# Performance work log

Hardware: AMD Instinct MI355X
Metric: run time of the kernel (lower is better)

## Reference

```python
import jax, jax.numpy as jnp
import numpy as np

N = 50000
E = 800000
IN_C = 128
HID = 64
HEADS = 4
NEG_SLOPE = 0.2
EPS = 1e-16


def setup_inputs() -> dict:
    key = jax.random.key(0)
    ks = jax.random.split(key, 12)
    x = jax.random.normal(ks[0], (N, IN_C), dtype=jnp.float32)
    edge_index = jax.random.randint(ks[1], (2, E), 0, N, dtype=jnp.int64)
    # layer 1: in -> (HEADS, HID), concat heads
    W1 = jax.random.normal(ks[2], (IN_C, HEADS * HID), dtype=jnp.float32) * (1.0 / np.sqrt(IN_C))
    a_src1 = jax.random.normal(ks[3], (HEADS, HID), dtype=jnp.float32) * 0.1
    a_dst1 = jax.random.normal(ks[4], (HEADS, HID), dtype=jnp.float32) * 0.1
    b1 = jnp.zeros((HEADS * HID,), dtype=jnp.float32)
    # layer 2: HEADS*HID -> (1, HID)
    W2 = jax.random.normal(ks[5], (HEADS * HID, HID), dtype=jnp.float32) * (1.0 / np.sqrt(HEADS * HID))
    a_src2 = jax.random.normal(ks[6], (1, HID), dtype=jnp.float32) * 0.1
    a_dst2 = jax.random.normal(ks[7], (1, HID), dtype=jnp.float32) * 0.1
    b2 = jnp.zeros((HID,), dtype=jnp.float32)
    return {"x": x, "edge_index": edge_index, "W1": W1, "a_src1": a_src1,
            "a_dst1": a_dst1, "b1": b1, "W2": W2, "a_src2": a_src2,
            "a_dst2": a_dst2, "b2": b2}


def _gat_conv(x, src, dst, W, a_src, a_dst, bias, heads, ch):
    n = x.shape[0]
    h = (x @ W).reshape(n, heads, ch)                       # [N,H,C]
    alpha_s = jnp.einsum('nhc,hc->nh', h, a_src)            # [N,H]
    alpha_d = jnp.einsum('nhc,hc->nh', h, a_dst)            # [N,H]
    e = jax.nn.leaky_relu(alpha_s[src] + alpha_d[dst], NEG_SLOPE)  # [E,H]
    # segment softmax over incoming edges of each dst node
    m = jax.ops.segment_max(e, dst, num_segments=n)         # [N,H]
    ex = jnp.exp(e - m[dst])
    denom = jax.ops.segment_sum(ex, dst, num_segments=n)    # [N,H]
    alpha = ex / (denom[dst] + EPS)                         # [E,H]
    msg = h[src] * alpha[:, :, None]                        # [E,H,C]
    out = jax.ops.segment_sum(msg, dst, num_segments=n)     # [N,H,C]
    return out.reshape(n, heads * ch) + bias


def reference(x, edge_index, W1, a_src1, a_dst1, b1, W2, a_src2, a_dst2, b2):
    src = edge_index[0]
    dst = edge_index[1]
    h = _gat_conv(x, src, dst, W1, a_src1, a_dst1, b1, HEADS, HID)
    h = jax.nn.elu(h)
    h = _gat_conv(h, src, dst, W2, a_src2, a_dst2, b2, 1, HID)
    h = jax.nn.elu(h)
    return h  # [N, HID] (output_dim == hidden_channels so no final linear)
```

## Files before the change

### kernel.cpp

```cpp
#include <hip/hip_runtime.h>
#include <math.h>

#define NN 50000
#define EE 800000
#define IN_C 128
#define HID 64
#define HEADS 4
#define SCAN_BLOCKS ((NN + 255) / 256)
#define EBLOCKS ((EE + 255) / 256)

typedef __attribute__((ext_vector_type(8))) short bf16x8;
typedef __attribute__((ext_vector_type(4))) float f32x4;

#if defined(__has_builtin)
#if __has_builtin(__builtin_amdgcn_fdot2_f32_bf16)
#define HAVE_FDOT2_BF16 1
#endif
#endif


__device__ inline unsigned short f2bf(float f) {
    unsigned u = __float_as_uint(f);
    return (unsigned short)((u + 0x7fff + ((u >> 16) & 1)) >> 16);
}
__device__ inline float bf2f(unsigned short s) {
    return __uint_as_float(((unsigned)s) << 16);
}
__device__ inline unsigned prm(unsigned a, unsigned b, unsigned sel) {
    return __builtin_amdgcn_perm(a, b, sel);
}
#ifdef HAVE_FDOT2_BF16
typedef __attribute__((ext_vector_type(2))) __bf16 bf2v;
__device__ inline float fdot2bf(unsigned h, unsigned w, float acc) {
    return __builtin_amdgcn_fdot2_f32_bf16(__builtin_bit_cast(bf2v, h),
                                           __builtin_bit_cast(bf2v, w), acc, false);
}
#else
__device__ inline float fdot2bf(unsigned h, unsigned w, float acc) {
    return acc + bf2f((unsigned short)(h & 0xffff)) * bf2f((unsigned short)(w & 0xffff))
               + bf2f((unsigned short)(h >> 16)) * bf2f((unsigned short)(w >> 16));
}
#endif

__device__ inline int wave_incl_scan(int v, int lane) {
    #pragma unroll
    for (int off = 1; off < 64; off <<= 1) {
        int t = __shfl_up(v, off);
        if (lane >= off) v += t;
    }
    return v;
}

__device__ inline int block256_excl_scan(int v, int tid, int* ws4) {
    int lane = tid & 63, wv = tid >> 6;
    int incl = wave_incl_scan(v, lane);
    if (lane == 63) ws4[wv] = incl;
    __syncthreads();
    if (tid == 0) {
        int run = 0;
        #pragma unroll
        for (int i = 0; i < 4; i++) { int t = ws4[i]; ws4[i] = run; run += t; }
    }
    __syncthreads();
    return incl + ws4[wv] - v;
}


__global__ void front_kernel(const int* __restrict__ ei, int* __restrict__ deg,
                             int* __restrict__ rank,
                             const float* __restrict__ W1, unsigned short* __restrict__ W1Thi,
                             unsigned short* __restrict__ W1Tlo,
                             const float* __restrict__ W2, unsigned short* __restrict__ W2Thi,
                             unsigned short* __restrict__ W2Tlo) {
    int b = blockIdx.x;
    int tid = threadIdx.x;
    if (b < EBLOCKS) {
        int i = b * 256 + tid;
        if (i < EE) rank[i] = atomicAdd(&deg[ei[EE + i]], 1);
    } else if (b < EBLOCKS + 128) {
        int idx = (b - EBLOCKS) * 256 + tid;
        int r = idx >> 8, c = idx & 255;
        float v = W1[idx];
        unsigned short h = f2bf(v);
        W1Thi[c * 128 + r] = h;
        W1Tlo[c * 128 + r] = f2bf(v - bf2f(h));
    } else {
        int idx = (b - EBLOCKS - 128) * 256 + tid;
        int r = idx >> 6, c = idx & 63;
        float v = W2[idx];
        unsigned short h = f2bf(v);
        W2Thi[c * 256 + r] = h;
        W2Tlo[c * 256 + r] = f2bf(v - bf2f(h));
    }
}


__global__ void deg_partial_kernel(const int* __restrict__ deg, int* __restrict__ bsum) {
    __shared__ int ws4[4];
    int tid = threadIdx.x;
    int idx = blockIdx.x * 256 + tid;
    int d = (idx < NN) ? deg[idx] : 0;
    int lane = tid & 63, wv = tid >> 6;
    int s = d;
    #pragma unroll
    for (int off = 32; off; off >>= 1) s += __shfl_down(s, off);
    if (lane == 0) ws4[wv] = s;
    __syncthreads();
    if (tid == 0) bsum[blockIdx.x] = ws4[0] + ws4[1] + ws4[2] + ws4[3];
}

__global__ void scanb_kernel(const int* __restrict__ bsum, int* __restrict__ boff,
                             int* __restrict__ row_ptr) {
    __shared__ int ws4[4];
    int tid = threadIdx.x;
    int v = (tid < SCAN_BLOCKS) ? bsum[tid] : 0;
    int excl = block256_excl_scan(v, tid, ws4);
    if (tid < SCAN_BLOCKS) boff[tid] = excl;
    if (tid == 255) row_ptr[NN] = excl + v;
}

__global__ void fill_kernel(const int* __restrict__ deg, const int* __restrict__ boff,
                            int* __restrict__ row_ptr) {
    __shared__ int ws4[4];
    int tid = threadIdx.x;
    int idx = blockIdx.x * 256 + tid;
    int d = (idx < NN) ? deg[idx] : 0;
    int excl = block256_excl_scan(d, tid, ws4) + boff[blockIdx.x];
    if (idx < NN) row_ptr[idx] = excl;
}

__global__ void scatter_kernel(const int* __restrict__ ei, const int* __restrict__ rank,
                               const int* __restrict__ row_ptr, int* __restrict__ csr_src) {
    int i = blockIdx.x * blockDim.x + threadIdx.x;
    if (i < EE) {
        int d = ei[EE + i];
        csr_src[row_ptr[d] + rank[i]] = ei[i];
    }
}

__global__ __launch_bounds__(256) void gemm1_mfma(
        const float* __restrict__ x,
        const unsigned short* __restrict__ Bhi, const unsigned short* __restrict__ Blo,
        const float* __restrict__ a_src, const float* __restrict__ a_dst,
        unsigned short* __restrict__ h1b, float* __restrict__ as1, float* __restrict__ ad1) {
    __shared__ unsigned short Ahi[32][136];
    __shared__ unsigned short Alo[32][136];
    int tid = threadIdx.x;
    int w = tid >> 6, lane = tid & 63;
    int lq = lane >> 4, lr = lane & 15;
    int brow = blockIdx.x * 32;
    {
        int row = tid >> 3;
        int col0 = (tid & 7) * 16;
        int gr = min(brow + row, NN - 1);
        #pragma unroll
        for (int i = 0; i < 16; i += 4) {
            float4 v = *(const float4*)(x + (size_t)gr * 128 + col0 + i);
            unsigned short h0 = f2bf(v.x), h1 = f2bf(v.y), h2 = f2bf(v.z), h3 = f2bf(v.w);
            Ahi[row][col0 + i + 0] = h0; Alo[row][col0 + i + 0] = f2bf(v.x - bf2f(h0));
            Ahi[row][col0 + i + 1] = h1; Alo[row][col0 + i + 1] = f2bf(v.y - bf2f(h1));
            Ahi[row][col0 + i + 2] = h2; Alo[row][col0 + i + 2] = f2bf(v.z - bf2f(h2));
            Ahi[row][col0 + i + 3] = h3; Alo[row][col0 + i + 3] = f2bf(v.w - bf2f(h3));
        }
    }
    __syncthreads();
    f32x4 acc[2][4];
    f32x4 zf = {0.f, 0.f, 0.f, 0.f};
    #pragma unroll
    for (int mi = 0; mi < 2; mi++)
        #pragma unroll
        for (int ni = 0; ni < 4; ni++) acc[mi][ni] = zf;
    #pragma unroll
    for (int q = 0; q < 4; q++) {
        int ko = q * 32 + lq * 8;
        bf16x8 ah0 = *(const bf16x8*)(const void*)&Ahi[lr][ko];
        bf16x8 al0 = *(const bf16x8*)(const void*)&Alo[lr][ko];
        bf16x8 ah1 = *(const bf16x8*)(const void*)&Ahi[16 + lr][ko];
        bf16x8 al1 = *(const bf16x8*)(const void*)&Alo[16 + lr][ko];
        #pragma unroll
        for (int ni = 0; ni < 4; ni++) {
            size_t bo = (size_t)(w * 64 + ni * 16 + lr) * 128 + ko;
            bf16x8 bh = *(const bf16x8*)(const void*)(Bhi + bo);
            bf16x8 bl = *(const bf16x8*)(const void*)(Blo + bo);
            acc[0][ni] = __builtin_amdgcn_mfma_f32_16x16x32_bf16(al0, bh, acc[0][ni], 0, 0, 0);
            acc[0][ni] = __builtin_amdgcn_mfma_f32_16x16x32_bf16(ah0, bl, acc[0][ni], 0, 0, 0);
            acc[0][ni] = __builtin_amdgcn_mfma_f32_16x16x32_bf16(ah0, bh, acc[0][ni], 0, 0, 0);
            acc[1][ni] = __builtin_amdgcn_mfma_f32_16x16x32_bf16(al1, bh, acc[1][ni], 0, 0, 0);
            acc[1][ni] = __builtin_amdgcn_mfma_f32_16x16x32_bf16(ah1, bl, acc[1][ni], 0, 0, 0);
            acc[1][ni] = __builtin_amdgcn_mfma_f32_16x16x32_bf16(ah1, bh, acc[1][ni], 0, 0, 0);
        }
    }
    float asv[4], adv[4];
    #pragma unroll
    for (int ni = 0; ni < 4; ni++) {
        asv[ni] = a_src[w * 64 + ni * 16 + lr];
        adv[ni] = a_dst[w * 64 + ni * 16 + lr];
    }
    #pragma unroll
    for (int mi = 0; mi < 2; mi++) {
        f32x4 ps = zf, pd = zf;
        #pragma unroll
        for (int ni = 0; ni < 4; ni++)
            #pragma unroll
            for (int r = 0; r < 4; r++) {
                ps[r] += acc[mi][ni][r] * asv[ni];
                pd[r] += acc[mi][ni][r] * adv[ni];
            }
        #pragma unroll
        for (int m = 1; m < 16; m <<= 1)
            #pragma unroll
            for (int r = 0; r < 4; r++) {
                ps[r] += __shfl_xor(ps[r], m);
                pd[r] += __shfl_xor(pd[r], m);
            }
        #pragma unroll
        for (int r = 0; r < 4; r++) {
            int n = brow + mi * 16 + lq * 4 + r;
            if (lr == 0 && n < NN) { as1[n * 4 + w] = ps[r]; ad1[n * 4 + w] = pd[r]; }
        }
        #pragma unroll
        for (int ni = 0; ni < 4; ni++)
            #pragma unroll
            for (int r = 0; r < 4; r++) {
                int n = brow + mi * 16 + lq * 4 + r;
                if (n < NN)
                    h1b[(size_t)n * 256 + w * 64 + ni * 16 + lr] = f2bf(acc[mi][ni][r]);
            }
    }
}

__global__ __launch_bounds__(256) void gemm2_mfma(
        const unsigned short* __restrict__ Ahi, const unsigned short* __restrict__ Alo,
        const unsigned short* __restrict__ Bhi, const unsigned short* __restrict__ Blo,
        const float* __restrict__ a_src, const float* __restrict__ a_dst,
        unsigned short* __restrict__ g2b, float* __restrict__ as2, float* __restrict__ ad2) {
    int tid = threadIdx.x;
    int w = tid >> 6, lane = tid & 63;
    int lq = lane >> 4, lr = lane & 15;
    int wrow = blockIdx.x * 128 + w * 32;
    f32x4 acc[2][4];
    f32x4 zf = {0.f, 0.f, 0.f, 0.f};
    #pragma unroll
    for (int mi = 0; mi < 2; mi++)
        #pragma unroll
        for (int ni = 0; ni < 4; ni++) acc[mi][ni] = zf;
    int ra = min(wrow + lr, NN - 1);
    int rb = min(wrow + 16 + lr, NN - 1);
    #pragma unroll
    for (int q = 0; q < 8; q++) {
        int ko = q * 32 + lq * 8;
        bf16x8 ah0 = *(const bf16x8*)(const void*)(Ahi + (size_t)ra * 256 + ko);
        bf16x8 al0 = *(const bf16x8*)(const void*)(Alo + (size_t)ra * 256 + ko);
        bf16x8 ah1 = *(const bf16x8*)(const void*)(Ahi + (size_t)rb * 256 + ko);
        bf16x8 al1 = *(const bf16x8*)(const void*)(Alo + (size_t)rb * 256 + ko);
        #pragma unroll
        for (int ni = 0; ni < 4; ni++) {
            size_t bo = (size_t)(ni * 16 + lr) * 256 + ko;
            bf16x8 bh = *(const bf16x8*)(const void*)(Bhi + bo);
            bf16x8 bl = *(const bf16x8*)(const void*)(Blo + bo);
            acc[0][ni] = __builtin_amdgcn_mfma_f32_16x16x32_bf16(al0, bh, acc[0][ni], 0, 0, 0);
            acc[0][ni] = __builtin_amdgcn_mfma_f32_16x16x32_bf16(ah0, bl, acc[0][ni], 0, 0, 0);
            acc[0][ni] = __builtin_amdgcn_mfma_f32_16x16x32_bf16(ah0, bh, acc[0][ni], 0, 0, 0);
            acc[1][ni] = __builtin_amdgcn_mfma_f32_16x16x32_bf16(al1, bh, acc[1][ni], 0, 0, 0);
            acc[1][ni] = __builtin_amdgcn_mfma_f32_16x16x32_bf16(ah1, bl, acc[1][ni], 0, 0, 0);
            acc[1][ni] = __builtin_amdgcn_mfma_f32_16x16x32_bf16(ah1, bh, acc[1][ni], 0, 0, 0);
        }
    }
    float asv[4], adv[4];
    #pragma unroll
    for (int ni = 0; ni < 4; ni++) {
        asv[ni] = a_src[ni * 16 + lr];
        adv[ni] = a_dst[ni * 16 + lr];
    }
    #pragma unroll
    for (int mi = 0; mi < 2; mi++) {
        f32x4 ps = zf, pd = zf;
        #pragma unroll
        for (int ni = 0; ni < 4; ni++)
            #pragma unroll
            for (int r = 0; r < 4; r++) {
                ps[r] += acc[mi][ni][r] * asv[ni];
                pd[r] += acc[mi][ni][r] * adv[ni];
            }
        #pragma unroll
        for (int m = 1; m < 16; m <<= 1)
            #pragma unroll
            for (int r = 0; r < 4; r++) {
                ps[r] += __shfl_xor(ps[r], m);
                pd[r] += __shfl_xor(pd[r], m);
            }
        #pragma unroll
        for (int r = 0; r < 4; r++) {
            int n = wrow + mi * 16 + lq * 4 + r;
            if (lr == 0 && n < NN) { as2[n] = ps[r]; ad2[n] = pd[r]; }
        }
        #pragma unroll
        for (int ni = 0; ni < 4; ni++)
            #pragma unroll
            for (int r = 0; r < 4; r++) {
                int n = wrow + mi * 16 + lq * 4 + r;
                if (n < NN)
                    g2b[(size_t)n * 64 + ni * 16 + lr] = f2bf(acc[mi][ni][r]);
            }
    }
}

__global__ __launch_bounds__(256) void agg1_kernel(
        const unsigned short* __restrict__ h1b, const int* __restrict__ row_ptr,
        const int* __restrict__ csr_src, const float* __restrict__ as,
        const float* __restrict__ ad, const float* __restrict__ b1,
        unsigned short* __restrict__ h2hi, unsigned short* __restrict__ h2lo) {
    __shared__ int            ssrc[4][64];
    __shared__ unsigned short wbf[4][4][64];
    int tid = threadIdx.x;
    int wv = tid >> 6, lane = tid & 63;
    int n = blockIdx.x * 4 + wv;
    if (n >= NN) return;
    int start = row_ptr[n], end = row_ptr[n + 1];
    float4 adv = ((const float4*)ad)[n];
    int whead = lane >> 4;
    float4 acc = make_float4(0.f, 0.f, 0.f, 0.f);
    float d0 = 0.f, d1 = 0.f, d2 = 0.f, d3 = 0.f;
    for (int c0 = start; c0 < end; c0 += 64) {
        int m = min(64, end - c0);
        if (lane < m) {
            int s = csr_src[c0 + lane];
            ssrc[wv][lane] = s;
            float4 asv = ((const float4*)as)[s];
            float e0 = asv.x + adv.x; e0 = e0 > 0.f ? e0 : 0.2f * e0; float x0 = __expf(e0);
            float e1 = asv.y + adv.y; e1 = e1 > 0.f ? e1 : 0.2f * e1; float x1 = __expf(e1);
            float e2 = asv.z + adv.z; e2 = e2 > 0.f ? e2 : 0.2f * e2; float x2 = __expf(e2);
            float e3 = asv.w + adv.w; e3 = e3 > 0.f ? e3 : 0.2f * e3; float x3 = __expf(e3);
            wbf[wv][0][lane] = f2bf(x0);
            wbf[wv][1][lane] = f2bf(x1);
            wbf[wv][2][lane] = f2bf(x2);
            wbf[wv][3][lane] = f2bf(x3);
            d0 += x0; d1 += x1; d2 += x2; d3 += x3;
        }
        int j = 0;
        for (; j + 4 <= m; j += 4) {
            int s0 = ssrc[wv][j], s1 = ssrc[wv][j + 1];
            int s2 = ssrc[wv][j + 2], s3 = ssrc[wv][j + 3];
            uint2 ha = ((const uint2*)h1b)[(size_t)s0 * 64 + lane];
            uint2 hb = ((const uint2*)h1b)[(size_t)s1 * 64 + lane];
            uint2 hc = ((const uint2*)h1b)[(size_t)s2 * 64 + lane];
            uint2 hd = ((const uint2*)h1b)[(size_t)s3 * 64 + lane];
            unsigned wp01 = *(const unsigned*)&wbf[wv][whead][j];
            unsigned wp23 = *(const unsigned*)&wbf[wv][whead][j + 2];
            acc.x = fdot2bf(prm(hb.x, ha.x, 0x05040100), wp01, acc.x);
            acc.y = fdot2bf(prm(hb.x, ha.x, 0x07060302), wp01, acc.y);
            acc.z = fdot2bf(prm(hb.y, ha.y, 0x05040100), wp01, acc.z);
            acc.w = fdot2bf(prm(hb.y, ha.y, 0x07060302), wp01, acc.w);
            acc.x = fdot2bf(prm(hd.x, hc.x, 0x05040100), wp23, acc.x);
            acc.y = fdot2bf(prm(hd.x, hc.x, 0x07060302), wp23, acc.y);
            acc.z = fdot2bf(prm(hd.y, hc.y, 0x05040100), wp23, acc.z);
            acc.w = fdot2bf(prm(hd.y, hc.y, 0x07060302), wp23, acc.w);
        }
        for (; j + 2 <= m; j += 2) {
            int s0 = ssrc[wv][j], s1 = ssrc[wv][j + 1];
            uint2 ha = ((const uint2*)h1b)[(size_t)s0 * 64 + lane];
            uint2 hb = ((const uint2*)h1b)[(size_t)s1 * 64 + lane];
            unsigned wp = *(const unsigned*)&wbf[wv][whead][j];
            acc.x = fdot2bf(prm(hb.x, ha.x, 0x05040100), wp, acc.x);
            acc.y = fdot2bf(prm(hb.x, ha.x, 0x07060302), wp, acc.y);
            acc.z = fdot2bf(prm(hb.y, ha.y, 0x05040100), wp, acc.z);
            acc.w = fdot2bf(prm(hb.y, ha.y, 0x07060302), wp, acc.w);
        }
        if (j < m) {
            int s = ssrc[wv][j];
            float w = bf2f(wbf[wv][whead][j]);
            ushort4 hv = ((const ushort4*)h1b)[(size_t)s * 64 + lane];
            acc.x += bf2f(hv.x) * w; acc.y += bf2f(hv.y) * w;
            acc.z += bf2f(hv.z) * w; acc.w += bf2f(hv.w) * w;
        }
    }
    #pragma unroll
    for (int off = 32; off; off >>= 1) {
        d0 += __shfl_down(d0, off); d1 += __shfl_down(d1, off);
        d2 += __shfl_down(d2, off); d3 += __shfl_down(d3, off);
    }
    d0 = __shfl(d0, 0); d1 = __shfl(d1, 0);
    d2 = __shfl(d2, 0); d3 = __shfl(d3, 0);
    float den = whead == 0 ? d0 : whead == 1 ? d1 : whead == 2 ? d2 : d3;
    float inv = 1.f / (den + 1e-16f);
    float4 bv = ((const float4*)b1)[lane];
    float4 r;
    r.x = acc.x * inv + bv.x; r.y = acc.y * inv + bv.y;
    r.z = acc.z * inv + bv.z; r.w = acc.w * inv + bv.w;
    r.x = r.x > 0.f ? r.x : expm1f(r.x);
    r.y = r.y > 0.f ? r.y : expm1f(r.y);
    r.z = r.z > 0.f ? r.z : expm1f(r.z);
    r.w = r.w > 0.f ? r.w : expm1f(r.w);
    ushort4 hi4, lo4;
    hi4.x = f2bf(r.x); lo4.x = f2bf(r.x - bf2f(hi4.x));
    hi4.y = f2bf(r.y); lo4.y = f2bf(r.y - bf2f(hi4.y));
    hi4.z = f2bf(r.z); lo4.z = f2bf(r.z - bf2f(hi4.z));
    hi4.w = f2bf(r.w); lo4.w = f2bf(r.w - bf2f(hi4.w));
    ((ushort4*)h2hi)[(size_t)n * 64 + lane] = hi4;
    ((ushort4*)h2lo)[(size_t)n * 64 + lane] = lo4;
}

__global__ __launch_bounds__(256) void agg2_kernel(
        const unsigned short* __restrict__ g2b, const int* __restrict__ row_ptr,
        const int* __restrict__ csr_src, const float* __restrict__ as,
        const float* __restrict__ ad, const float* __restrict__ b2,
        float* __restrict__ out) {
    __shared__ int            ssrc[4][64];
    __shared__ unsigned short wbf[4][64];
    int tid = threadIdx.x;
    int wv = tid >> 6, lane = tid & 63;
    int n = blockIdx.x * 4 + wv;
    if (n >= NN) return;
    int start = row_ptr[n], end = row_ptr[n + 1];
    float adv = ad[n];
    float acc = 0.f;
    float den = 0.f;
    for (int c0 = start; c0 < end; c0 += 64) {
        int m = min(64, end - c0);
        if (lane < m) {
            int s = csr_src[c0 + lane];
            ssrc[wv][lane] = s;
            float e = as[s] + adv;
            e = e > 0.f ? e : 0.2f * e;
            float x = __expf(e);
            wbf[wv][lane] = f2bf(x);
            den += x;
        }
        int j = 0;
        for (; j + 4 <= m; j += 4) {
            int s0 = ssrc[wv][j], s1 = ssrc[wv][j + 1];
            int s2 = ssrc[wv][j + 2], s3 = ssrc[wv][j + 3];
            unsigned g0 = g2b[(size_t)s0 * 64 + lane];
            unsigned g1 = g2b[(size_t)s1 * 64 + lane];
            unsigned g2 = g2b[(size_t)s2 * 64 + lane];
            unsigned g3 = g2b[(size_t)s3 * 64 + lane];
            unsigned wp01 = *(const unsigned*)&wbf[wv][j];
            unsigned wp23 = *(const unsigned*)&wbf[wv][j + 2];
            acc = fdot2bf(prm(g1, g0, 0x05040100), wp01, acc);
            acc = fdot2bf(prm(g3, g2, 0x05040100), wp23, acc);
        }
        for (; j + 2 <= m; j += 2) {
            int s0 = ssrc[wv][j], s1 = ssrc[wv][j + 1];
            unsigned g0 = g2b[(size_t)s0 * 64 + lane];
            unsigned g1 = g2b[(size_t)s1 * 64 + lane];
            unsigned wp = *(const unsigned*)&wbf[wv][j];
            acc = fdot2bf(prm(g1, g0, 0x05040100), wp, acc);
        }
        if (j < m) {
            int s = ssrc[wv][j];
            acc += bf2f(g2b[(size_t)s * 64 + lane]) * bf2f(wbf[wv][j]);
        }
    }
    #pragma unroll
    for (int off = 32; off; off >>= 1) den += __shfl_down(den, off);
    den = __shfl(den, 0);
    float inv = 1.f / (den + 1e-16f);
    float r = acc * inv + b2[lane];
    out[(size_t)n * 64 + lane] = r > 0.f ? r : expm1f(r);
}


extern "C" void kernel_launch(void* const* d_in, const int* in_sizes, int n_in,
                              void* d_out, int out_size, void* d_ws, size_t ws_size,
                              hipStream_t stream) {
    const float* x      = (const float*)d_in[0];
    const int*   ei     = (const int*)d_in[1];
    const float* W1     = (const float*)d_in[2];
    const float* a_src1 = (const float*)d_in[3];
    const float* a_dst1 = (const float*)d_in[4];
    const float* b1     = (const float*)d_in[5];
    const float* W2     = (const float*)d_in[6];
    const float* a_src2 = (const float*)d_in[7];
    const float* a_dst2 = (const float*)d_in[8];
    const float* b2     = (const float*)d_in[9];
    float* out = (float*)d_out;

    char* base = (char*)d_ws;
    size_t off = 0;
    auto alloc = [&](size_t bytes) -> void* {
        void* p = base + off;
        off = (off + bytes + 255) & ~(size_t)255;
        return p;
    };
    int*   deg     = (int*)alloc(NN * sizeof(int));
    int*   rank    = (int*)alloc(EE * sizeof(int));
    int*   bsum    = (int*)alloc(SCAN_BLOCKS * sizeof(int));
    int*   boff    = (int*)alloc(SCAN_BLOCKS * sizeof(int));
    int*   row_ptr = (int*)alloc((NN + 1) * sizeof(int));
    int*   csr_src = (int*)alloc(EE * sizeof(int));
    unsigned short* W1Thi = (unsigned short*)alloc(256 * 128 * 2);
    unsigned short* W1Tlo = (unsigned short*)alloc(256 * 128 * 2);
    unsigned short* W2Thi = (unsigned short*)alloc(64 * 256 * 2);
    unsigned short* W2Tlo = (unsigned short*)alloc(64 * 256 * 2);
    unsigned short* h1b   = (unsigned short*)alloc((size_t)NN * 256 * 2);
    float* as1     = (float*)alloc((size_t)NN * 4 * sizeof(float));
    float* ad1     = (float*)alloc((size_t)NN * 4 * sizeof(float));
    unsigned short* h2hi  = (unsigned short*)alloc((size_t)NN * 256 * 2);
    unsigned short* h2lo  = (unsigned short*)alloc((size_t)NN * 256 * 2);
    unsigned short* g2b   = (unsigned short*)alloc((size_t)NN * 64 * 2);
    float* as2     = (float*)alloc((size_t)NN * sizeof(float));
    float* ad2     = (float*)alloc((size_t)NN * sizeof(float));

    hipMemsetAsync(deg, 0, NN * sizeof(int), stream);

    front_kernel<<<EBLOCKS + 128 + 64, 256, 0, stream>>>(ei, deg, rank, W1, W1Thi, W1Tlo,
                                                         W2, W2Thi, W2Tlo);
    deg_partial_kernel<<<SCAN_BLOCKS, 256, 0, stream>>>(deg, bsum);
    scanb_kernel<<<1, 256, 0, stream>>>(bsum, boff, row_ptr);
    fill_kernel<<<SCAN_BLOCKS, 256, 0, stream>>>(deg, boff, row_ptr);
    scatter_kernel<<<EBLOCKS, 256, 0, stream>>>(ei, rank, row_ptr, csr_src);

    gemm1_mfma<<<(NN + 31) / 32, 256, 0, stream>>>(x, W1Thi, W1Tlo,
                                                   a_src1, a_dst1, h1b, as1, ad1);
    agg1_kernel<<<(NN + 3) / 4, 256, 0, stream>>>(h1b, row_ptr, csr_src, as1, ad1, b1,
                                                  h2hi, h2lo);
    gemm2_mfma<<<(NN + 127) / 128, 256, 0, stream>>>(h2hi, h2lo, W2Thi, W2Tlo,
                                                     a_src2, a_dst2, g2b, as2, ad2);
    agg2_kernel<<<(NN + 3) / 4, 256, 0, stream>>>(g2b, row_ptr, csr_src, as2, ad2, b2, out);
}
```

Before: 291.9 us.

## Fuse CSR scan into single-pass lookback, enlarge gemm1 tile, drop h2 lo split

Replaces the three-kernel degree scan with one kernel that uses per-block descriptors and a decoupled lookback, which removes two launches. gemm1 now processes 64 rows per block instead of 32 so each B fragment load feeds more MFMAs. The layer-1 output is stored only as a bf16 hi part, and gemm2 drops the lo MFMA terms for A, cutting one 25 MB write, one read and a third of the gemm2 MFMAs. The cost is lower precision in layer 2's input, plus a lookback that depends on earlier blocks being scheduled first.

```diff
diff --git a/kernel.cpp b/kernel.cpp
--- a/kernel.cpp
+++ b/kernel.cpp
@@ -94,39 +94,44 @@
     }
 }
 
-
-__global__ void deg_partial_kernel(const int* __restrict__ deg, int* __restrict__ bsum) {
+__global__ void scan_fill_kernel(const int* __restrict__ deg,
+                                 unsigned long long* __restrict__ desc,
+                                 int* __restrict__ row_ptr) {
     __shared__ int ws4[4];
-    int tid = threadIdx.x;
-    int idx = blockIdx.x * 256 + tid;
+    __shared__ int sbase;
+    int b = blockIdx.x, tid = threadIdx.x;
+    int idx = b * 256 + tid;
     int d = (idx < NN) ? deg[idx] : 0;
-    int lane = tid & 63, wv = tid >> 6;
-    int s = d;
-    #pragma unroll
-    for (int off = 32; off; off >>= 1) s += __shfl_down(s, off);
-    if (lane == 0) ws4[wv] = s;
+    int excl = block256_excl_scan(d, tid, ws4);
+    if (tid == 255) {
+        unsigned total = (unsigned)(excl + d);
+        __threadfence();
+        atomicExch(&desc[b], (1ULL << 32) | (unsigned long long)total);
+    }
+    if (tid < 64) {
+        int sum = 0;
+        int hi = b;
+        while (hi > 0) {
+            int lo = hi - 64; if (lo < 0) lo = 0;
+            int myi = lo + tid;
+            unsigned v = 0;
+            if (myi < hi) {
+                unsigned long long d8;
+                do { d8 = atomicAdd(&desc[myi], 0ULL); } while ((d8 >> 32) == 0);
+                v = (unsigned)(d8 & 0xffffffffULL);
+            }
+            #pragma unroll
+            for (int off = 32; off; off >>= 1) v += __shfl_down(v, off);
+            v = __shfl(v, 0);
+            sum += (int)v;
+            hi = lo;
+        }
+        if (tid == 0) sbase = sum;
+    }
     __syncthreads();
-    if (tid == 0) bsum[blockIdx.x] = ws4[0] + ws4[1] + ws4[2] + ws4[3];
-}
-
-__global__ void scanb_kernel(const int* __restrict__ bsum, int* __restrict__ boff,
-                             int* __restrict__ row_ptr) {
-    __shared__ int ws4[4];
-    int tid = threadIdx.x;
-    int v = (tid < SCAN_BLOCKS) ? bsum[tid] : 0;
-    int excl = block256_excl_scan(v, tid, ws4);
-    if (tid < SCAN_BLOCKS) boff[tid] = excl;
-    if (tid == 255) row_ptr[NN] = excl + v;
-}
-
-__global__ void fill_kernel(const int* __restrict__ deg, const int* __restrict__ boff,
-                            int* __restrict__ row_ptr) {
-    __shared__ int ws4[4];
-    int tid = threadIdx.x;
-    int idx = blockIdx.x * 256 + tid;
-    int d = (idx < NN) ? deg[idx] : 0;
-    int excl = block256_excl_scan(d, tid, ws4) + boff[blockIdx.x];
-    if (idx < NN) row_ptr[idx] = excl;
+    int gbase = sbase;
+    if (idx < NN) row_ptr[idx] = gbase + excl;
+    if (b == gridDim.x - 1 && tid == 255) row_ptr[NN] = gbase + excl + d;
 }
 
 __global__ void scatter_kernel(const int* __restrict__ ei, const int* __restrict__ rank,
@@ -143,18 +148,18 @@
         const unsigned short* __restrict__ Bhi, const unsigned short* __restrict__ Blo,
         const float* __restrict__ a_src, const float* __restrict__ a_dst,
         unsigned short* __restrict__ h1b, float* __restrict__ as1, float* __restrict__ ad1) {
-    __shared__ unsigned short Ahi[32][136];
-    __shared__ unsigned short Alo[32][136];
+    __shared__ unsigned short Ahi[64][136];
+    __shared__ unsigned short Alo[64][136];
     int tid = threadIdx.x;
     int w = tid >> 6, lane = tid & 63;
     int lq = lane >> 4, lr = lane & 15;
-    int brow = blockIdx.x * 32;
+    int brow = blockIdx.x * 64;
     {
-        int row = tid >> 3;
-        int col0 = (tid & 7) * 16;
+        int row = tid >> 2;
+        int col0 = (tid & 3) * 32;
         int gr = min(brow + row, NN - 1);
         #pragma unroll
-        for (int i = 0; i < 16; i += 4) {
+        for (int i = 0; i < 32; i += 4) {
             float4 v = *(const float4*)(x + (size_t)gr * 128 + col0 + i);
             unsigned short h0 = f2bf(v.x), h1 = f2bf(v.y), h2 = f2bf(v.z), h3 = f2bf(v.w);
             Ahi[row][col0 + i + 0] = h0; Alo[row][col0 + i + 0] = f2bf(v.x - bf2f(h0));
@@ -164,30 +169,32 @@
         }
     }
     __syncthreads();
-    f32x4 acc[2][4];
+    f32x4 acc[4][4];
     f32x4 zf = {0.f, 0.f, 0.f, 0.f};
     #pragma unroll
-    for (int mi = 0; mi < 2; mi++)
+    for (int mi = 0; mi < 4; mi++)
         #pragma unroll
         for (int ni = 0; ni < 4; ni++) acc[mi][ni] = zf;
     #pragma unroll
     for (int q = 0; q < 4; q++) {
         int ko = q * 32 + lq * 8;
-        bf16x8 ah0 = *(const bf16x8*)(const void*)&Ahi[lr][ko];
-        bf16x8 al0 = *(const bf16x8*)(const void*)&Alo[lr][ko];
-        bf16x8 ah1 = *(const bf16x8*)(const void*)&Ahi[16 + lr][ko];
-        bf16x8 al1 = *(const bf16x8*)(const void*)&Alo[16 + lr][ko];
+        bf16x8 ah[4], al[4];
+        #pragma unroll
+        for (int mi = 0; mi < 4; mi++) {
+            ah[mi] = *(const bf16x8*)(const void*)&Ahi[mi * 16 + lr][ko];
+            al[mi] = *(const bf16x8*)(const void*)&Alo[mi * 16 + lr][ko];
+        }
         #pragma unroll
         for (int ni = 0; ni < 4; ni++) {
             size_t bo = (size_t)(w * 64 + ni * 16 + lr) * 128 + ko;
             bf16x8 bh = *(const bf16x8*)(const void*)(Bhi + bo);
             bf16x8 bl = *(const bf16x8*)(const void*)(Blo + bo);
-            acc[0][ni] = __builtin_amdgcn_mfma_f32_16x16x32_bf16(al0, bh, acc[0][ni], 0, 0, 0);
-            acc[0][ni] = __builtin_amdgcn_mfma_f32_16x16x32_bf16(ah0, bl, acc[0][ni], 0, 0, 0);
-            acc[0][ni] = __builtin_amdgcn_mfma_f32_16x16x32_bf16(ah0, bh, acc[0][ni], 0, 0, 0);
-            acc[1][ni] = __builtin_amdgcn_mfma_f32_16x16x32_bf16(al1, bh, acc[1][ni], 0, 0, 0);
-            acc[1][ni] = __builtin_amdgcn_mfma_f32_16x16x32_bf16(ah1, bl, acc[1][ni], 0, 0, 0);
-            acc[1][ni] = __builtin_amdgcn_mfma_f32_16x16x32_bf16(ah1, bh, acc[1][ni], 0, 0, 0);
+            #pragma unroll
+            for (int mi = 0; mi < 4; mi++) {
+                acc[mi][ni] = __builtin_amdgcn_mfma_f32_16x16x32_bf16(al[mi], bh, acc[mi][ni], 0, 0, 0);
+                acc[mi][ni] = __builtin_amdgcn_mfma_f32_16x16x32_bf16(ah[mi], bl, acc[mi][ni], 0, 0, 0);
+                acc[mi][ni] = __builtin_amdgcn_mfma_f32_16x16x32_bf16(ah[mi], bh, acc[mi][ni], 0, 0, 0);
+            }
         }
     }
     float asv[4], adv[4];
@@ -197,7 +204,7 @@
         adv[ni] = a_dst[w * 64 + ni * 16 + lr];
     }
     #pragma unroll
-    for (int mi = 0; mi < 2; mi++) {
+    for (int mi = 0; mi < 4; mi++) {
         f32x4 ps = zf, pd = zf;
         #pragma unroll
         for (int ni = 0; ni < 4; ni++)
@@ -230,7 +237,7 @@
 }
 
 __global__ __launch_bounds__(256) void gemm2_mfma(
-        const unsigned short* __restrict__ Ahi, const unsigned short* __restrict__ Alo,
+        const unsigned short* __restrict__ Ab,
         const unsigned short* __restrict__ Bhi, const unsigned short* __restrict__ Blo,
         const float* __restrict__ a_src, const float* __restrict__ a_dst,
         unsigned short* __restrict__ g2b, float* __restrict__ as2, float* __restrict__ ad2) {
@@ -249,19 +256,15 @@
     #pragma unroll
     for (int q = 0; q < 8; q++) {
         int ko = q * 32 + lq * 8;
-        bf16x8 ah0 = *(const bf16x8*)(const void*)(Ahi + (size_t)ra * 256 + ko);
-        bf16x8 al0 = *(const bf16x8*)(const void*)(Alo + (size_t)ra * 256 + ko);
-        bf16x8 ah1 = *(const bf16x8*)(const void*)(Ahi + (size_t)rb * 256 + ko);
-        bf16x8 al1 = *(const bf16x8*)(const void*)(Alo + (size_t)rb * 256 + ko);
+        bf16x8 ah0 = *(const bf16x8*)(const void*)(Ab + (size_t)ra * 256 + ko);
+        bf16x8 ah1 = *(const bf16x8*)(const void*)(Ab + (size_t)rb * 256 + ko);
         #pragma unroll
         for (int ni = 0; ni < 4; ni++) {
             size_t bo = (size_t)(ni * 16 + lr) * 256 + ko;
             bf16x8 bh = *(const bf16x8*)(const void*)(Bhi + bo);
             bf16x8 bl = *(const bf16x8*)(const void*)(Blo + bo);
-            acc[0][ni] = __builtin_amdgcn_mfma_f32_16x16x32_bf16(al0, bh, acc[0][ni], 0, 0, 0);
             acc[0][ni] = __builtin_amdgcn_mfma_f32_16x16x32_bf16(ah0, bl, acc[0][ni], 0, 0, 0);
             acc[0][ni] = __builtin_amdgcn_mfma_f32_16x16x32_bf16(ah0, bh, acc[0][ni], 0, 0, 0);
-            acc[1][ni] = __builtin_amdgcn_mfma_f32_16x16x32_bf16(al1, bh, acc[1][ni], 0, 0, 0);
             acc[1][ni] = __builtin_amdgcn_mfma_f32_16x16x32_bf16(ah1, bl, acc[1][ni], 0, 0, 0);
             acc[1][ni] = __builtin_amdgcn_mfma_f32_16x16x32_bf16(ah1, bh, acc[1][ni], 0, 0, 0);
         }
@@ -309,7 +312,7 @@
         const unsigned short* __restrict__ h1b, const int* __restrict__ row_ptr,
         const int* __restrict__ csr_src, const float* __restrict__ as,
         const float* __restrict__ ad, const float* __restrict__ b1,
-        unsigned short* __restrict__ h2hi, unsigned short* __restrict__ h2lo) {
+        unsigned short* __restrict__ h2b) {
     __shared__ int            ssrc[4][64];
     __shared__ unsigned short wbf[4][4][64];
     int tid = threadIdx.x;
@@ -391,13 +394,9 @@
     r.y = r.y > 0.f ? r.y : expm1f(r.y);
     r.z = r.z > 0.f ? r.z : expm1f(r.z);
     r.w = r.w > 0.f ? r.w : expm1f(r.w);
-    ushort4 hi4, lo4;
-    hi4.x = f2bf(r.x); lo4.x = f2bf(r.x - bf2f(hi4.x));
-    hi4.y = f2bf(r.y); lo4.y = f2bf(r.y - bf2f(hi4.y));
-    hi4.z = f2bf(r.z); lo4.z = f2bf(r.z - bf2f(hi4.z));
-    hi4.w = f2bf(r.w); lo4.w = f2bf(r.w - bf2f(hi4.w));
-    ((ushort4*)h2hi)[(size_t)n * 64 + lane] = hi4;
-    ((ushort4*)h2lo)[(size_t)n * 64 + lane] = lo4;
+    ushort4 hv;
+    hv.x = f2bf(r.x); hv.y = f2bf(r.y); hv.z = f2bf(r.z); hv.w = f2bf(r.w);
+    ((ushort4*)h2b)[(size_t)n * 64 + lane] = hv;
 }
 
 __global__ __launch_bounds__(256) void agg2_kernel(
@@ -483,9 +482,8 @@
         return p;
     };
     int*   deg     = (int*)alloc(NN * sizeof(int));
+    unsigned long long* desc = (unsigned long long*)alloc(SCAN_BLOCKS * sizeof(unsigned long long));
     int*   rank    = (int*)alloc(EE * sizeof(int));
-    int*   bsum    = (int*)alloc(SCAN_BLOCKS * sizeof(int));
-    int*   boff    = (int*)alloc(SCAN_BLOCKS * sizeof(int));
     int*   row_ptr = (int*)alloc((NN + 1) * sizeof(int));
     int*   csr_src = (int*)alloc(EE * sizeof(int));
     unsigned short* W1Thi = (unsigned short*)alloc(256 * 128 * 2);
@@ -495,26 +493,23 @@
     unsigned short* h1b   = (unsigned short*)alloc((size_t)NN * 256 * 2);
     float* as1     = (float*)alloc((size_t)NN * 4 * sizeof(float));
     float* ad1     = (float*)alloc((size_t)NN * 4 * sizeof(float));
-    unsigned short* h2hi  = (unsigned short*)alloc((size_t)NN * 256 * 2);
-    unsigned short* h2lo  = (unsigned short*)alloc((size_t)NN * 256 * 2);
+    unsigned short* h2b   = (unsigned short*)alloc((size_t)NN * 256 * 2);
     unsigned short* g2b   = (unsigned short*)alloc((size_t)NN * 64 * 2);
     float* as2     = (float*)alloc((size_t)NN * sizeof(float));
     float* ad2     = (float*)alloc((size_t)NN * sizeof(float));
 
-    hipMemsetAsync(deg, 0, NN * sizeof(int), stream);
+    size_t clear_bytes = (size_t)((char*)(desc + SCAN_BLOCKS) - (char*)deg);
+    hipMemsetAsync(deg, 0, clear_bytes, stream);
 
     front_kernel<<<EBLOCKS + 128 + 64, 256, 0, stream>>>(ei, deg, rank, W1, W1Thi, W1Tlo,
                                                          W2, W2Thi, W2Tlo);
-    deg_partial_kernel<<<SCAN_BLOCKS, 256, 0, stream>>>(deg, bsum);
-    scanb_kernel<<<1, 256, 0, stream>>>(bsum, boff, row_ptr);
-    fill_kernel<<<SCAN_BLOCKS, 256, 0, stream>>>(deg, boff, row_ptr);
+    scan_fill_kernel<<<SCAN_BLOCKS, 256, 0, stream>>>(deg, desc, row_ptr);
     scatter_kernel<<<EBLOCKS, 256, 0, stream>>>(ei, rank, row_ptr, csr_src);
 
-    gemm1_mfma<<<(NN + 31) / 32, 256, 0, stream>>>(x, W1Thi, W1Tlo,
+    gemm1_mfma<<<(NN + 63) / 64, 256, 0, stream>>>(x, W1Thi, W1Tlo,
                                                    a_src1, a_dst1, h1b, as1, ad1);
-    agg1_kernel<<<(NN + 3) / 4, 256, 0, stream>>>(h1b, row_ptr, csr_src, as1, ad1, b1,
-                                                  h2hi, h2lo);
-    gemm2_mfma<<<(NN + 127) / 128, 256, 0, stream>>>(h2hi, h2lo, W2Thi, W2Tlo,
+    agg1_kernel<<<(NN + 3) / 4, 256, 0, stream>>>(h1b, row_ptr, csr_src, as1, ad1, b1, h2b);
+    gemm2_mfma<<<(NN + 127) / 128, 256, 0, stream>>>(h2b, W2Thi, W2Tlo,
                                                      a_src2, a_dst2, g2b, as2, ad2);
     agg2_kernel<<<(NN + 3) / 4, 256, 0, stream>>>(g2b, row_ptr, csr_src, as2, ad2, b2, out);
 }
```

After: 287.7 us. About the same (-1.4%).
